# Performance work log

Hardware: AMD Instinct MI355X
Metric: run time of the kernel (lower is better)

Reference implementation:

```python
import jax, jax.numpy as jnp
import numpy as np

L, B, N, C, H = 8, 8, 512, 1024, 16
D = C // H
TP = (2.0 * D) ** 0.5  # temperature_coeff * head_dim, sqrt


def _ln(x):
    # LayerNorm(eps=1e-6, no affine)
    m = jnp.mean(x, axis=-1, keepdims=True)
    v = jnp.var(x, axis=-1, keepdims=True)
    return (x - m) * jax.lax.rsqrt(v + 1e-6)


def _modulate(x, shift, scale):
    return x * (1 + scale) + shift


def setup_inputs() -> dict:
    key = jax.random.key(0)
    ks = jax.random.split(key, 18)
    s = 0.02
    return {
        "x": jax.random.normal(ks[0], (B, N, C), dtype=jnp.float32),
        "time": jax.random.uniform(ks[1], (B, 1), dtype=jnp.float32) * 100.0,
        "label": jax.random.normal(ks[2], (B, 2), dtype=jnp.float32),
        "x_mask": jax.random.randint(ks[3], (B, N, 1), 0, 2).astype(jnp.float32),
        # ValueLabelEmbed: Linear(2 -> C)
        "Wl": jax.random.normal(ks[4], (C, 2), dtype=jnp.float32) * s,
        "bl": jnp.zeros((C,), dtype=jnp.float32),
        # per-layer stacked weights (leading dim L)
        "Wq": jax.random.normal(ks[5], (L, C, C), dtype=jnp.float32) * s,
        "Wk": jax.random.normal(ks[6], (L, C, C), dtype=jnp.float32) * s,
        "Wv": jax.random.normal(ks[7], (L, C, C), dtype=jnp.float32) * s,
        "W1": jax.random.normal(ks[8], (L, 4 * C, C), dtype=jnp.float32) * s,
        "b1": jnp.zeros((L, 4 * C), dtype=jnp.float32),
        "W2": jax.random.normal(ks[9], (L, C, 4 * C), dtype=jnp.float32) * s,
        "b2": jnp.zeros((L, C), dtype=jnp.float32),
        "Wm": jax.random.normal(ks[10], (L, 6 * C, C), dtype=jnp.float32) * s,
        "bm": jnp.zeros((L, 6 * C), dtype=jnp.float32),
        # FinalLayer
        "Wf": jax.random.normal(ks[11], (C, C), dtype=jnp.float32) * s,
        "bf": jnp.zeros((C,), dtype=jnp.float32),
        "Wmf": jax.random.normal(ks[12], (2 * C, C), dtype=jnp.float32) * s,
        "bmf": jnp.zeros((2 * C,), dtype=jnp.float32),
    }


def reference(x, time, label, x_mask, Wl, bl, Wq, Wk, Wv, W1, b1, W2, b2, Wm, bm, Wf, bf, Wmf, bmf):
    # ValueLabelEmbed: (B,2) -> (B,1,C)
    lemb = (label @ Wl.T + bl)[:, None, :]
    # TimeEmbedding: interleaved sin/cos of time / 10000^(2i/d)
    base = jnp.power(10000.0, 2.0 * jnp.arange(C, dtype=jnp.float32) / C)
    te = time / base  # (B, C)
    even = (jnp.arange(C) % 2) == 0
    te = jnp.where(even, jnp.sin(te), jnp.cos(te))
    c = lemb + te[:, None, :]  # (B,1,C)

    # self-attention mask: True where exactly one of the pair is valid
    xm = x_mask[:, :, 0]  # (B,N)
    mask = ((xm[:, :, None] + xm[:, None, :]) == 1.0)[:, None, :, :]  # (B,1,N,N)

    def block(xc, p):
        wq, wk, wv, w1, bb1, w2, bb2, wm, bbm = p
        m6 = jax.nn.selu(c) @ wm.T + bbm  # (B,1,6C)
        sm, sc, gm, sf, cf, gf = jnp.split(m6, 6, axis=-1)
        h = _modulate(_ln(xc), sm, sc) * x_mask
        q = (h @ wq.T).reshape(B, N, H, D)
        k = (h @ wk.T).reshape(B, N, H, D)
        v = (h @ wv.T).reshape(B, N, H, D)
        scores = jnp.einsum('bqhd,bkhd->bhqk', q, k) / TP
        scores = jnp.where(mask, -jnp.inf, scores)
        alpha = jax.nn.softmax(scores, axis=-1)
        att = jnp.einsum('bhqk,bkhd->bqhd', alpha, v).reshape(B, N, C)
        xc = xc + gm * att
        h2 = _modulate(_ln(xc), sf, cf)
        ffn = jax.nn.selu(h2 @ w1.T + bb1) @ w2.T + bb2
        xc = (xc + gf * ffn) * x_mask
        return xc, None

    x, _ = jax.lax.scan(block, x, (Wq, Wk, Wv, W1, b1, W2, b2, Wm, bm))

    # FinalLayer
    m2 = jax.nn.selu(c) @ Wmf.T + bmf
    shift, scale = jnp.split(m2, 2, axis=-1)
    out = (_modulate(_ln(x), shift, scale) @ Wf.T + bf) * x_mask
    return out
```

## Files before the change

kernel.cpp:

```cpp
#include <hip/hip_runtime.h>
#include <hip/hip_bf16.h>
#include <cstddef>

#define DEVI __device__ __forceinline__

typedef __attribute__((ext_vector_type(4))) float f4v;
typedef __attribute__((ext_vector_type(8))) short s8v;
typedef __attribute__((ext_vector_type(4))) short s4v;

using bf16 = __hip_bfloat16;

constexpr float SELU_A = 1.6732632423543772f;
constexpr float SELU_S = 1.0507009873554805f;
constexpr float TPINV  = 0.08838834764831845f;

DEVI float bfbits(short s) { return __uint_as_float(((unsigned)(unsigned short)s) << 16); }
DEVI unsigned short f2bu(float f) {
  bf16 h = __float2bfloat16(f);
  return __builtin_bit_cast(unsigned short, h);
}
DEVI float seluf(float x) { return x > 0.f ? SELU_S * x : SELU_S * SELU_A * (__expf(x) - 1.f); }

DEVI void gl16(const void* g, void* l) {
  __builtin_amdgcn_global_load_lds((__attribute__((address_space(1))) void*)g,
                                   (__attribute__((address_space(3))) void*)l, 16, 0, 0);
}

DEVI void conv8(const float* __restrict__ src, bf16* __restrict__ dst) {
  f4v a = *(const f4v*)src;
  f4v b = *(const f4v*)(src + 4);
  s8v o;
  #pragma unroll
  for (int j = 0; j < 4; j++) { o[j] = (short)f2bu(a[j]); o[4 + j] = (short)f2bu(b[j]); }
  *(s8v*)dst = o;
}

__global__ void k_compact(const float* __restrict__ xm, int* __restrict__ idx,
                          int* __restrict__ pos, int* __restrict__ cnt,
                          int* __restrict__ start, int* __restrict__ t2b)
{
  int t = threadIdx.x;
  int b = t >> 6, lane = t & 63;
  __shared__ int scnt[8];
  int base = b * 512 + lane * 8;
  int mb[8]; int lc = 0;
  #pragma unroll
  for (int i = 0; i < 8; i++) { mb[i] = (xm[base + i] != 0.f) ? 1 : 0; lc += mb[i]; }
  int s = lc;
  #pragma unroll
  for (int o = 1; o < 64; o <<= 1) { int tt = __shfl_up(s, o); if (lane >= o) s += tt; }
  int run = s - lc;
  #pragma unroll
  for (int i = 0; i < 8; i++) {
    int n = lane * 8 + i;
    if (mb[i]) { idx[b * 512 + run] = n; pos[b * 512 + n] = run; run++; }
    else pos[b * 512 + n] = -1;
  }
  if (lane == 63) scnt[b] = s;
  __syncthreads();
  if (t == 0) {
    int st = 0, tile = 0;
    for (int bb = 0; bb < 8; bb++) {
      cnt[bb] = scnt[bb];
      start[bb] = st;
      int nt = (scnt[bb] + 127) >> 7;
      for (int k = 0; k < nt; k++) t2b[tile++] = bb;
      st += nt * 128;
    }
    start[8] = st;
    for (; tile < 32; tile++) t2b[tile] = 0;
  }
}

__global__ __launch_bounds__(256) void k_gather(const float* __restrict__ xin,
    const int* __restrict__ idx, const int* __restrict__ cnt,
    const int* __restrict__ start, const int* __restrict__ t2b,
    float* __restrict__ xc)
{
  int row = blockIdx.x, t = threadIdx.x;
  if (row >= start[8]) return;
  int tb = t2b[row >> 7], slot = row - start[tb];
  f4v v = {0.f, 0.f, 0.f, 0.f};
  if (slot < cnt[tb])
    v = *(const f4v*)&xin[((size_t)tb * 512 + idx[tb * 512 + slot]) * 1024 + t * 4];
  *(f4v*)&xc[(size_t)row * 1024 + t * 4] = v;
}

__global__ __launch_bounds__(256) void k_scatter(const float* __restrict__ ffin,
    const int* __restrict__ pos, const int* __restrict__ start, float* __restrict__ out)
{
  int row = blockIdx.x, t = threadIdx.x, b = row >> 9;
  int p = pos[row];
  f4v v = {0.f, 0.f, 0.f, 0.f};
  if (p >= 0) v = *(const f4v*)&ffin[(size_t)(start[b] + p) * 1024 + t * 4];
  *(f4v*)&out[(size_t)row * 1024 + t * 4] = v;
}

__global__ __launch_bounds__(256) void k_convall(
    const float* __restrict__ wq, const float* __restrict__ wk, const float* __restrict__ wv,
    const float* __restrict__ w1, const float* __restrict__ w2,
    bf16* __restrict__ wqkvb, bf16* __restrict__ w1b, bf16* __restrict__ w2b)
{
  int i = blockIdx.x * 256 + threadIdx.x;
  if (i < 393216) {
    int o = i * 8;
    int row = o >> 10, col = o & 1023;
    int sel = row >> 10, sr = row & 1023;
    conv8((sel == 0 ? wq : sel == 1 ? wk : wv) + (size_t)sr * 1024 + col, wqkvb + o);
  } else if (i < 917504) {
    size_t o = (size_t)(i - 393216) * 8;
    conv8(w1 + o, w1b + o);
  } else if (i < 1441792) {
    size_t o = (size_t)(i - 917504) * 8;
    conv8(w2 + o, w2b + o);
  }
}

__global__ void k_cond(const float* __restrict__ tim, const float* __restrict__ lab,
                       const float* __restrict__ Wl, const float* __restrict__ bl,
                       float* __restrict__ cs)
{
  int b = blockIdx.x, t = threadIdx.x;
  float l0 = lab[b * 2 + 0], l1 = lab[b * 2 + 1], tv = tim[b];
  #pragma unroll
  for (int i = 0; i < 4; i++) {
    int j = t + 256 * i;
    float e = powf(10000.f, (2.f * (float)j) * (1.f / 1024.f));
    float arg = tv / e;
    float te = ((j & 1) == 0) ? sinf(arg) : cosf(arg);
    float c = l0 * Wl[j * 2 + 0] + l1 * Wl[j * 2 + 1] + bl[j] + te;
    cs[b * 1024 + j] = seluf(c);
  }
}

__global__ __launch_bounds__(256) void k_small(
    const float* __restrict__ cs, const float* __restrict__ W, const float* __restrict__ bias,
    float* __restrict__ out, int O, int mode)
{
  __shared__ float cls[8192];
  int t = threadIdx.x;
  #pragma unroll
  for (int i = 0; i < 8; i++)
    *(f4v*)&cls[i * 1024 + t * 4] = *(const f4v*)&cs[i * 1024 + t * 4];
  __syncthreads();
  int w = t >> 6, l = t & 63;
  int o = blockIdx.x * 4 + w;
  if (o >= O) return;
  float acc[8] = {0.f, 0.f, 0.f, 0.f, 0.f, 0.f, 0.f, 0.f};
  const float* Wr = W + (size_t)o * 1024;
  for (int i = 0; i < 16; i++) {
    int k = i * 64 + l;
    float wv = Wr[k];
    #pragma unroll
    for (int b = 0; b < 8; b++) acc[b] += wv * cls[b * 1024 + k];
  }
  #pragma unroll
  for (int b = 0; b < 8; b++) {
    #pragma unroll
    for (int off = 32; off; off >>= 1) acc[b] += __shfl_xor(acc[b], off);
  }
  float bv = bias[o];
  #pragma unroll
  for (int b = 0; b < 8; b++) {
    if (l == b) {
      float val = acc[b] + bv;
      size_t dst;
      if (mode == 0) { int ll = o / 6144, ft = o - ll * 6144; dst = ((size_t)ll * 8 + b) * 6144 + ft; }
      else dst = (size_t)b * 2048 + o;
      out[dst] = val;
    }
  }
}

__global__ __launch_bounds__(256) void k_lnmod(
    const float* __restrict__ x, const float* __restrict__ shiftB, const float* __restrict__ scaleB,
    int bstride, const int* __restrict__ cnt, const int* __restrict__ start,
    const int* __restrict__ t2b, bf16* __restrict__ out)
{
  int row = blockIdx.x, t = threadIdx.x;
  if (row >= start[8]) return;
  int tb = t2b[row >> 7], slot = row - start[tb];
  if (slot >= cnt[tb]) {
    s4v z = {0, 0, 0, 0};
    *(s4v*)&out[(size_t)row * 1024 + t * 4] = z;
    return;
  }
  const float* xr = x + (size_t)row * 1024;
  f4v v = *(const f4v*)&xr[t * 4];
  float s = v[0] + v[1] + v[2] + v[3];
  float ss = v[0]*v[0] + v[1]*v[1] + v[2]*v[2] + v[3]*v[3];
  #pragma unroll
  for (int off = 32; off; off >>= 1) { s += __shfl_xor(s, off); ss += __shfl_xor(ss, off); }
  __shared__ float rs[4], rss[4];
  int w = t >> 6;
  if ((t & 63) == 0) { rs[w] = s; rss[w] = ss; }
  __syncthreads();
  s = rs[0] + rs[1] + rs[2] + rs[3];
  ss = rss[0] + rss[1] + rss[2] + rss[3];
  float mean = s * (1.f / 1024.f);
  float var = ss * (1.f / 1024.f) - mean * mean;
  float rstd = rsqrtf(var + 1e-6f);
  f4v sh = *(const f4v*)&shiftB[(size_t)tb * bstride + t * 4];
  f4v sc = *(const f4v*)&scaleB[(size_t)tb * bstride + t * 4];
  s4v o;
  #pragma unroll
  for (int i = 0; i < 4; i++)
    o[i] = (short)f2bu((v[i] - mean) * rstd * (1.f + sc[i]) + sh[i]);
  *(s4v*)&out[(size_t)row * 1024 + t * 4] = o;
}

__global__ __launch_bounds__(256) void k_resid(
    float* __restrict__ x, const bf16* __restrict__ att, const float* __restrict__ m6b,
    const int* __restrict__ cnt, const int* __restrict__ start,
    const int* __restrict__ t2b, bf16* __restrict__ h2)
{
  int row = blockIdx.x, t = threadIdx.x;
  if (row >= start[8]) return;
  int tb = t2b[row >> 7], slot = row - start[tb];
  if (slot >= cnt[tb]) {
    s4v z = {0, 0, 0, 0};
    *(s4v*)&h2[(size_t)row * 1024 + t * 4] = z;
    return;
  }
  float* xr = x + (size_t)row * 1024;
  const float* gm = m6b + (size_t)tb * 6144 + 2048;
  const float* sf = m6b + (size_t)tb * 6144 + 3072;
  const float* cf = m6b + (size_t)tb * 6144 + 4096;
  f4v xv = *(const f4v*)&xr[t * 4];
  s4v av = *(const s4v*)&att[((size_t)tb * 512 + slot) * 1024 + t * 4];
  f4v gv = *(const f4v*)&gm[t * 4];
  f4v vv;
  #pragma unroll
  for (int i = 0; i < 4; i++) vv[i] = xv[i] + gv[i] * bfbits(av[i]);
  *(f4v*)&xr[t * 4] = vv;
  float s = vv[0] + vv[1] + vv[2] + vv[3];
  float ss = vv[0]*vv[0] + vv[1]*vv[1] + vv[2]*vv[2] + vv[3]*vv[3];
  #pragma unroll
  for (int off = 32; off; off >>= 1) { s += __shfl_xor(s, off); ss += __shfl_xor(ss, off); }
  __shared__ float rs[4], rss[4];
  int w = t >> 6;
  if ((t & 63) == 0) { rs[w] = s; rss[w] = ss; }
  __syncthreads();
  s = rs[0] + rs[1] + rs[2] + rs[3];
  ss = rss[0] + rss[1] + rss[2] + rss[3];
  float mean = s * (1.f / 1024.f);
  float var = ss * (1.f / 1024.f) - mean * mean;
  float rstd = rsqrtf(var + 1e-6f);
  f4v sfv = *(const f4v*)&sf[t * 4];
  f4v cfv = *(const f4v*)&cf[t * 4];
  s4v o;
  #pragma unroll
  for (int i = 0; i < 4; i++)
    o[i] = (short)f2bu((vv[i] - mean) * rstd * (1.f + cfv[i]) + sfv[i]);
  *(s4v*)&h2[(size_t)row * 1024 + t * 4] = o;
}

__global__ __launch_bounds__(256) void k_attn(
    const bf16* __restrict__ q, const bf16* __restrict__ k, const bf16* __restrict__ vt,
    const int* __restrict__ cnt, bf16* __restrict__ att,
    const float* __restrict__ nwq, const float* __restrict__ nwk, const float* __restrict__ nwv,
    const float* __restrict__ nw1, const float* __restrict__ nw2,
    bf16* __restrict__ dqkv, bf16* __restrict__ dw1, bf16* __restrict__ dw2, int mode)
{
  if (blockIdx.x >= 4) {
    int cid = (blockIdx.x - 4) * 128 + blockIdx.y;
    int i0 = cid * 256 + threadIdx.x;
    #pragma unroll
    for (int half = 0; half < 2; half++) {
      int j = i0 * 2 + half;
      if (mode == 1) {
        if (j < 131072) conv8(nwq + (size_t)j * 8, dqkv + (size_t)j * 8);
      } else {
        if (j < 393216) {
          int o = j * 8;
          int row = o >> 10, col = o & 1023;
          int sel = row >> 10, sr = row & 1023;
          conv8((sel == 0 ? nwq : sel == 1 ? nwk : nwv) + (size_t)sr * 1024 + col, dqkv + o);
        } else if (j < 917504) {
          size_t o = (size_t)(j - 393216) * 8;
          conv8(nw1 + o, dw1 + o);
        } else {
          size_t o = (size_t)(j - 917504) * 8;
          conv8(nw2 + o, dw2 + o);
        }
      }
    }
    return;
  }

  int bh = blockIdx.y, b = bh >> 4, hh = bh & 15;
  int cntb = cnt[b];
  if ((int)blockIdx.x * 128 >= cntb) return;
  int t = threadIdx.x, w = t >> 6, lane = t & 63;
  int fr = lane & 15, g = lane >> 4;
  int qw = blockIdx.x * 128 + w * 32;
  const size_t ho = (size_t)bh * (512 * 64);

  __shared__ bf16 Pb[4][32][72];

  s8v qf[2][2];
  #pragma unroll
  for (int mf = 0; mf < 2; mf++)
    #pragma unroll
    for (int kk = 0; kk < 2; kk++)
      qf[mf][kk] = *(const s8v*)(q + ho + (size_t)(qw + mf * 16 + fr) * 64 + kk * 32 + g * 8);

  float mrow[2][4], lsum[2][4];
  f4v oacc[2][4];
  const f4v vzero = {0.f, 0.f, 0.f, 0.f};
  #pragma unroll
  for (int mf = 0; mf < 2; mf++)
    #pragma unroll
    for (int r = 0; r < 4; r++) { mrow[mf][r] = -3.0e38f; lsum[mf][r] = 0.f; }
  #pragma unroll
  for (int mf = 0; mf < 2; mf++)
    #pragma unroll
    for (int nd = 0; nd < 4; nd++) oacc[mf][nd] = vzero;

  int nkt = (cntb + 63) >> 6;
  for (int kt = 0; kt < nkt; kt++) {
    int kb0 = kt * 64;
    f4v sacc[2][4];
    #pragma unroll
    for (int mf = 0; mf < 2; mf++)
      #pragma unroll
      for (int nf = 0; nf < 4; nf++) sacc[mf][nf] = vzero;
    #pragma unroll
    for (int kk = 0; kk < 2; kk++) {
      s8v kf[4];
      #pragma unroll
      for (int nf = 0; nf < 4; nf++)
        kf[nf] = *(const s8v*)(k + ho + (size_t)(kb0 + nf * 16 + fr) * 64 + kk * 32 + g * 8);
      #pragma unroll
      for (int mf = 0; mf < 2; mf++)
        #pragma unroll
        for (int nf = 0; nf < 4; nf++)
          sacc[mf][nf] = __builtin_amdgcn_mfma_f32_16x16x32_bf16(qf[mf][kk], kf[nf], sacc[mf][nf], 0, 0, 0);
    }
    #pragma unroll
    for (int mf = 0; mf < 2; mf++) {
      #pragma unroll
      for (int r = 0; r < 4; r++) {
        float mx = -3.0e38f;
        #pragma unroll
        for (int nf = 0; nf < 4; nf++) {
          float s = sacc[mf][nf][r] * TPINV;
          if (kb0 + nf * 16 + fr >= cntb) s = -1.0e30f;
          sacc[mf][nf][r] = s;
          mx = fmaxf(mx, s);
        }
        mx = fmaxf(mx, __shfl_xor(mx, 1));
        mx = fmaxf(mx, __shfl_xor(mx, 2));
        mx = fmaxf(mx, __shfl_xor(mx, 4));
        mx = fmaxf(mx, __shfl_xor(mx, 8));
        float mnew = fmaxf(mrow[mf][r], mx);
        float corr = __expf(mrow[mf][r] - mnew);
        mrow[mf][r] = mnew;
        float ps = 0.f;
        #pragma unroll
        for (int nf = 0; nf < 4; nf++) {
          float p = __expf(sacc[mf][nf][r] - mnew);
          ps += p;
          Pb[w][mf * 16 + g * 4 + r][nf * 16 + fr] = __float2bfloat16(p);
        }
        lsum[mf][r] = lsum[mf][r] * corr + ps;
        #pragma unroll
        for (int nd = 0; nd < 4; nd++) oacc[mf][nd][r] *= corr;
      }
    }
    #pragma unroll
    for (int kk = 0; kk < 2; kk++) {
      s8v pf[2], vf[4];
      #pragma unroll
      for (int mf = 0; mf < 2; mf++)
        pf[mf] = *(const s8v*)&Pb[w][mf * 16 + fr][kk * 32 + g * 8];
      #pragma unroll
      for (int nd = 0; nd < 4; nd++)
        vf[nd] = *(const s8v*)(vt + ho + (size_t)(nd * 16 + fr) * 512 + kb0 + kk * 32 + g * 8);
      #pragma unroll
      for (int mf = 0; mf < 2; mf++)
        #pragma unroll
        for (int nd = 0; nd < 4; nd++)
          oacc[mf][nd] = __builtin_amdgcn_mfma_f32_16x16x32_bf16(pf[mf], vf[nd], oacc[mf][nd], 0, 0, 0);
    }
  }
  float inv[2][4];
  #pragma unroll
  for (int mf = 0; mf < 2; mf++)
    #pragma unroll
    for (int r = 0; r < 4; r++) {
      float ls = lsum[mf][r];
      ls += __shfl_xor(ls, 1);
      ls += __shfl_xor(ls, 2);
      ls += __shfl_xor(ls, 4);
      ls += __shfl_xor(ls, 8);
      inv[mf][r] = 1.f / ls;
    }
  #pragma unroll
  for (int mf = 0; mf < 2; mf++)
    #pragma unroll
    for (int nd = 0; nd < 4; nd++)
      #pragma unroll
      for (int r = 0; r < 4; r++) {
        int row = qw + mf * 16 + g * 4 + r;
        att[(size_t)(b * 512 + row) * 1024 + hh * 64 + nd * 16 + fr] =
            __float2bfloat16(oacc[mf][nd][r] * inv[mf][r]);
      }
}

template <int EPI, int BN>
__global__ __launch_bounds__(256) void k_gemm(
    const bf16* __restrict__ A, const bf16* __restrict__ W,
    const float* __restrict__ bias, int Kst, int kLen, int Ncols,
    const int* __restrict__ cnt, const int* __restrict__ start, const int* __restrict__ t2b,
    bf16* __restrict__ outb, float* __restrict__ outf)
{
  constexpr int FN = BN / 32;
  constexpr int NW = BN / 32;
  __shared__ bf16 As[128][64];
  __shared__ bf16 Ws[BN][64];
  int t = threadIdx.x, lane = t & 63, w = t >> 6;
  int wr = w >> 1, wc = w & 1;
  int m0 = blockIdx.y * 128, n0 = blockIdx.x * BN;
  if (m0 >= start[8]) return;
  int kOff = blockIdx.z * kLen;
  int fr = lane & 15, g = lane >> 4;

  const bf16* Abase = A + (size_t)m0 * Kst + kOff;
  const bf16* Wbase = W + (size_t)n0 * Kst + kOff;

  const f4v vzero = {0.f, 0.f, 0.f, 0.f};
  f4v acc[4][FN];
  #pragma unroll
  for (int i = 0; i < 4; i++)
    #pragma unroll
    for (int j = 0; j < FN; j++) acc[i][j] = vzero;

  int nkt = kLen >> 6;
  for (int kt = 0; kt < nkt; kt++) {
    int k0 = kt << 6;
    __syncthreads();
    #pragma unroll
    for (int i = 0; i < 4; i++) {
      int off = w * 4096 + i * 1024 + lane * 16;
      int row = off >> 7, ce = (off & 127) >> 1;
      gl16(Abase + (size_t)row * Kst + k0 + ce, (char*)As + w * 4096 + i * 1024);
    }
    #pragma unroll
    for (int i = 0; i < NW; i++) {
      int off = w * (NW * 1024) + i * 1024 + lane * 16;
      int row = off >> 7, ce = (off & 127) >> 1;
      gl16(Wbase + (size_t)row * Kst + k0 + ce, (char*)Ws + w * (NW * 1024) + i * 1024);
    }
    __syncthreads();
    #pragma unroll
    for (int kk = 0; kk < 2; kk++) {
      s8v af[4], bfr[FN];
      #pragma unroll
      for (int mf = 0; mf < 4; mf++)
        af[mf] = *(const s8v*)&As[wr * 64 + mf * 16 + fr][kk * 32 + g * 8];
      #pragma unroll
      for (int nf = 0; nf < FN; nf++)
        bfr[nf] = *(const s8v*)&Ws[wc * (BN / 2) + nf * 16 + fr][kk * 32 + g * 8];
      #pragma unroll
      for (int mf = 0; mf < 4; mf++)
        #pragma unroll
        for (int nf = 0; nf < FN; nf++)
          acc[mf][nf] = __builtin_amdgcn_mfma_f32_16x16x32_bf16(af[mf], bfr[nf], acc[mf][nf], 0, 0, 0);
    }
  }

  int tb = t2b[m0 >> 7];
  int sb = start[tb];
  int rq = (lane >> 4) * 4;
  #pragma unroll
  for (int mf = 0; mf < 4; mf++) {
    #pragma unroll
    for (int nf = 0; nf < FN; nf++) {
      int row0 = m0 + wr * 64 + mf * 16 + rq;
      int col = n0 + wc * (BN / 2) + nf * 16 + fr;
      if (EPI == 0) {
        int sel = col >> 10, cl = col & 1023;
        int nn = row0 - sb;
        int h2 = cl >> 6, dd = cl & 63;
        if (sel == 2) {
          s4v o4;
          #pragma unroll
          for (int r = 0; r < 4; r++) o4[r] = (short)f2bu(acc[mf][nf][r]);
          *(s4v*)&outb[(size_t)2 * 4194304 + (((size_t)tb * 16 + h2) * 64 + dd) * 512 + nn] = o4;
        } else {
          #pragma unroll
          for (int r = 0; r < 4; r++)
            outb[(size_t)sel * 4194304 + (((size_t)tb * 16 + h2) * 512 + (nn + r)) * 64 + dd] =
                __float2bfloat16(acc[mf][nf][r]);
        }
      } else {
        #pragma unroll
        for (int r = 0; r < 4; r++) {
          int row = row0 + r;
          float val = acc[mf][nf][r];
          if (EPI == 1) {
            outb[(size_t)row * Ncols + col] = __float2bfloat16(seluf(val + bias[col]));
          } else if (EPI == 3) {
            outf[(size_t)row * 1024 + col] = val + bias[col];
          } else {
            outb[(size_t)blockIdx.z * 4194304 + (size_t)row * 1024 + col] = __float2bfloat16(val);
          }
        }
      }
    }
  }
}

__global__ __launch_bounds__(256) void k_comb(
    const bf16* __restrict__ part, const float* __restrict__ bias,
    const float* __restrict__ gfb, const float* __restrict__ shiftN,
    const float* __restrict__ scaleN, int strideN,
    float* __restrict__ x, const int* __restrict__ cnt, const int* __restrict__ start,
    const int* __restrict__ t2b, bf16* __restrict__ h)
{
  int row = blockIdx.x, t = threadIdx.x;
  if (row >= start[8]) return;
  int tb = t2b[row >> 7], slot = row - start[tb];
  if (slot >= cnt[tb]) return;
  size_t o = (size_t)row * 1024 + t * 4;
  f4v sum = {0.f, 0.f, 0.f, 0.f};
  #pragma unroll
  for (int p = 0; p < 8; p++) {
    s4v pv = *(const s4v*)&part[o + (size_t)p * 4194304];
    #pragma unroll
    for (int i = 0; i < 4; i++) sum[i] += bfbits(pv[i]);
  }
  f4v bv = *(const f4v*)&bias[t * 4];
  f4v gf = *(const f4v*)&gfb[(size_t)tb * 6144 + t * 4];
  f4v xv = *(const f4v*)&x[o];
  f4v vv;
  #pragma unroll
  for (int i = 0; i < 4; i++)
    vv[i] = xv[i] + gf[i] * (sum[i] + bv[i]);
  *(f4v*)&x[o] = vv;
  float s = vv[0] + vv[1] + vv[2] + vv[3];
  float ss = vv[0]*vv[0] + vv[1]*vv[1] + vv[2]*vv[2] + vv[3]*vv[3];
  #pragma unroll
  for (int off = 32; off; off >>= 1) { s += __shfl_xor(s, off); ss += __shfl_xor(ss, off); }
  __shared__ float rs[4], rss[4];
  int w = t >> 6;
  if ((t & 63) == 0) { rs[w] = s; rss[w] = ss; }
  __syncthreads();
  s = rs[0] + rs[1] + rs[2] + rs[3];
  ss = rss[0] + rss[1] + rss[2] + rss[3];
  float mean = s * (1.f / 1024.f);
  float var = ss * (1.f / 1024.f) - mean * mean;
  float rstd = rsqrtf(var + 1e-6f);
  f4v sh = *(const f4v*)&shiftN[(size_t)tb * strideN + t * 4];
  f4v sc = *(const f4v*)&scaleN[(size_t)tb * strideN + t * 4];
  s4v ho;
  #pragma unroll
  for (int i = 0; i < 4; i++)
    ho[i] = (short)f2bu((vv[i] - mean) * rstd * (1.f + sc[i]) + sh[i]);
  *(s4v*)&h[(size_t)row * 1024 + t * 4] = ho;
}

extern "C" void kernel_launch(void* const* d_in, const int* in_sizes, int n_in,
                              void* d_out, int out_size, void* d_ws, size_t ws_size,
                              hipStream_t stream)
{
  const float* x_in  = (const float*)d_in[0];
  const float* tim   = (const float*)d_in[1];
  const float* lab   = (const float*)d_in[2];
  const float* xmask = (const float*)d_in[3];
  const float* Wl  = (const float*)d_in[4];
  const float* bl  = (const float*)d_in[5];
  const float* Wq  = (const float*)d_in[6];
  const float* Wk  = (const float*)d_in[7];
  const float* Wv  = (const float*)d_in[8];
  const float* W1  = (const float*)d_in[9];
  const float* b1  = (const float*)d_in[10];
  const float* W2  = (const float*)d_in[11];
  const float* b2  = (const float*)d_in[12];
  const float* Wm  = (const float*)d_in[13];
  const float* bm  = (const float*)d_in[14];
  const float* Wf  = (const float*)d_in[15];
  const float* bfp = (const float*)d_in[16];
  const float* Wmf = (const float*)d_in[17];
  const float* bmf = (const float*)d_in[18];

  char* ws = (char*)d_ws;
  float* x     = (float*)(ws + 0);
  float* cs    = (float*)(ws + 16777216);
  float* mAll  = (float*)(ws + 16809984);
  float* m2v   = (float*)(ws + 18382848);
  bf16*  h     = (bf16*)(ws + 18448384);
  bf16*  qb    = (bf16*)(ws + 26836992);
  bf16*  kb    = (bf16*)(ws + 35225600);
  bf16*  vb    = (bf16*)(ws + 43614208);
  bf16*  att   = (bf16*)(ws + 52002816);
  bf16*  f1    = (bf16*)(ws + 60391424);
  bf16*  wqkv0 = (bf16*)(ws + 93945856);
  bf16*  w1b0  = (bf16*)(ws + 100237312);
  bf16*  w2b0  = (bf16*)(ws + 108625920);
  bf16*  wfb   = (bf16*)(ws + 117014528);
  float* ffin  = (float*)(ws + 119111680);
  int*   idxb  = (int*)(ws + 135888896);
  int*   posb  = (int*)(ws + 135905280);
  int*   cntb  = (int*)(ws + 135921664);
  int*   strtb = (int*)(ws + 135921728);
  int*   t2bb  = (int*)(ws + 135921792);
  bf16*  wqkv1 = (bf16*)(ws + 135921920);
  bf16*  w1b1  = (bf16*)(ws + 142213376);
  bf16*  w2b1  = (bf16*)(ws + 150601984);
  bf16*  part  = (bf16*)(ws + 158990592);

  bf16* wqkvS[2] = { wqkv0, wqkv1 };
  bf16* w1S[2]   = { w1b0, w1b1 };
  bf16* w2S[2]   = { w2b0, w2b1 };

  k_compact<<<1, 512, 0, stream>>>(xmask, idxb, posb, cntb, strtb, t2bb);
  k_gather<<<4096, 256, 0, stream>>>(x_in, idxb, cntb, strtb, t2bb, x);

  k_cond<<<8, 256, 0, stream>>>(tim, lab, Wl, bl, cs);
  k_small<<<12288, 256, 0, stream>>>(cs, Wm, bm, mAll, 49152, 0);
  k_small<<<512, 256, 0, stream>>>(cs, Wmf, bmf, m2v, 2048, 1);

  k_convall<<<5632, 256, 0, stream>>>(Wq, Wk, Wv, W1, W2, wqkv0, w1b0, w2b0);
  k_lnmod<<<4096, 256, 0, stream>>>(x, mAll + 0, mAll + 1024, 6144, cntb, strtb, t2bb, h);

  for (int l = 0; l < 8; l++) {
    const float* m6b = mAll + (size_t)l * 49152;
    int sel = l & 1, nsel = sel ^ 1;
    int last = (l == 7);

    k_gemm<0, 64><<<dim3(48, 32), 256, 0, stream>>>(h, wqkvS[sel], nullptr, 1024, 1024, 3072,
                                                    cntb, strtb, t2bb, qb, nullptr);
    if (!last) {
      k_attn<<<dim3(26, 128), 256, 0, stream>>>(qb, kb, vb, cntb, att,
          Wq + (size_t)(l + 1) * 1048576, Wk + (size_t)(l + 1) * 1048576,
          Wv + (size_t)(l + 1) * 1048576, W1 + (size_t)(l + 1) * 4194304,
          W2 + (size_t)(l + 1) * 4194304,
          wqkvS[nsel], w1S[nsel], w2S[nsel], 0);
    } else {
      k_attn<<<dim3(26, 128), 256, 0, stream>>>(qb, kb, vb, cntb, att,
          Wf, Wf, Wf, Wf, Wf, wfb, wfb, wfb, 1);
    }
    k_resid<<<4096, 256, 0, stream>>>(x, att, m6b, cntb, strtb, t2bb, h);
    k_gemm<1, 64><<<dim3(64, 32), 256, 0, stream>>>(h, w1S[sel], b1 + l * 4096, 1024, 1024, 4096,
                                                    cntb, strtb, t2bb, f1, nullptr);
    k_gemm<4, 128><<<dim3(8, 32, 8), 256, 0, stream>>>(f1, w2S[sel], nullptr, 4096, 512, 1024,
                                                       cntb, strtb, t2bb, part, nullptr);
    const float* nShift = last ? m2v : (mAll + (size_t)(l + 1) * 49152);
    const float* nScale = last ? (m2v + 1024) : (mAll + (size_t)(l + 1) * 49152 + 1024);
    int nStride = last ? 2048 : 6144;
    k_comb<<<4096, 256, 0, stream>>>(part, b2 + l * 1024, m6b + 5120,
                                     nShift, nScale, nStride,
                                     x, cntb, strtb, t2bb, h);
  }

  k_gemm<3, 64><<<dim3(16, 32), 256, 0, stream>>>(h, wfb, bfp, 1024, 1024, 1024,
                                                  cntb, strtb, t2bb, nullptr, ffin);
  k_scatter<<<4096, 256, 0, stream>>>(ffin, posb, strtb, (float*)d_out);
}
```

Measured before the change: 1.500 ms.

## Switch GEMM to 32x32x16 MFMA with XOR-swizzled LDS tiles

The generic GEMM kernel now issues 32x32x16 bf16 MFMA instructions instead of 16x16x32, so each wave handles two 32-row fragments per N fragment. LDS tiles are stored with an XOR swizzle on 16-byte slots, keyed by row, both when filling from global memory and when reading fragments, to avoid bank conflicts. The epilogue is remapped to the 32x32 accumulator layout (four quads of four rows). This aims to cut LDS read conflicts and per-FLOP instruction overhead. The risk is mis-mapping the output or swizzle layout, and BN must be a multiple of 64.

```diff
diff --git a/kernel.cpp b/kernel.cpp
--- a/kernel.cpp
+++ b/kernel.cpp
@@ -5,6 +5,7 @@
 #define DEVI __device__ __forceinline__
 
 typedef __attribute__((ext_vector_type(4))) float f4v;
+typedef __attribute__((ext_vector_type(16))) float f16v;
 typedef __attribute__((ext_vector_type(8))) short s8v;
 typedef __attribute__((ext_vector_type(4))) short s4v;
 
@@ -415,8 +416,8 @@
     const int* __restrict__ cnt, const int* __restrict__ start, const int* __restrict__ t2b,
     bf16* __restrict__ outb, float* __restrict__ outf)
 {
-  constexpr int FN = BN / 32;
-  constexpr int NW = BN / 32;
+  constexpr int NFR = BN / 64;
+  constexpr int NW  = BN / 32;
   __shared__ bf16 As[128][64];
   __shared__ bf16 Ws[BN][64];
   int t = threadIdx.x, lane = t & 63, w = t >> 6;
@@ -424,17 +425,18 @@
   int m0 = blockIdx.y * 128, n0 = blockIdx.x * BN;
   if (m0 >= start[8]) return;
   int kOff = blockIdx.z * kLen;
-  int fr = lane & 15, g = lane >> 4;
+  int r32 = lane & 31, hi = lane >> 5;
 
   const bf16* Abase = A + (size_t)m0 * Kst + kOff;
   const bf16* Wbase = W + (size_t)n0 * Kst + kOff;
 
-  const f4v vzero = {0.f, 0.f, 0.f, 0.f};
-  f4v acc[4][FN];
-  #pragma unroll
-  for (int i = 0; i < 4; i++)
-    #pragma unroll
-    for (int j = 0; j < FN; j++) acc[i][j] = vzero;
+  f16v acc[2][NFR];
+  #pragma unroll
+  for (int i = 0; i < 2; i++)
+    #pragma unroll
+    for (int j = 0; j < NFR; j++)
+      #pragma unroll
+      for (int e = 0; e < 16; e++) acc[i][j][e] = 0.f;
 
   int nkt = kLen >> 6;
   for (int kt = 0; kt < nkt; kt++) {
@@ -442,69 +444,79 @@
     __syncthreads();
     #pragma unroll
     for (int i = 0; i < 4; i++) {
-      int off = w * 4096 + i * 1024 + lane * 16;
-      int row = off >> 7, ce = (off & 127) >> 1;
-      gl16(Abase + (size_t)row * Kst + k0 + ce, (char*)As + w * 4096 + i * 1024);
+      int Z = w * 4096 + i * 1024 + lane * 16;
+      int row = Z >> 7, slot = (Z >> 4) & 7;
+      int ss = slot ^ (row & 7);
+      gl16(Abase + (size_t)row * Kst + k0 + ss * 8, (char*)As + Z);
     }
     #pragma unroll
     for (int i = 0; i < NW; i++) {
-      int off = w * (NW * 1024) + i * 1024 + lane * 16;
-      int row = off >> 7, ce = (off & 127) >> 1;
-      gl16(Wbase + (size_t)row * Kst + k0 + ce, (char*)Ws + w * (NW * 1024) + i * 1024);
+      int Z = w * (NW * 1024) + i * 1024 + lane * 16;
+      int row = Z >> 7, slot = (Z >> 4) & 7;
+      int ss = slot ^ (row & 7);
+      gl16(Wbase + (size_t)row * Kst + k0 + ss * 8, (char*)Ws + Z);
     }
     __syncthreads();
     #pragma unroll
-    for (int kk = 0; kk < 2; kk++) {
-      s8v af[4], bfr[FN];
-      #pragma unroll
-      for (int mf = 0; mf < 4; mf++)
-        af[mf] = *(const s8v*)&As[wr * 64 + mf * 16 + fr][kk * 32 + g * 8];
-      #pragma unroll
-      for (int nf = 0; nf < FN; nf++)
-        bfr[nf] = *(const s8v*)&Ws[wc * (BN / 2) + nf * 16 + fr][kk * 32 + g * 8];
-      #pragma unroll
-      for (int mf = 0; mf < 4; mf++)
+    for (int kk = 0; kk < 4; kk++) {
+      s8v af[2], bfr[NFR];
+      #pragma unroll
+      for (int mf = 0; mf < 2; mf++) {
+        int row = wr * 64 + mf * 32 + r32;
+        int sl = (kk * 2 + hi) ^ (row & 7);
+        af[mf] = *(const s8v*)((const char*)As + row * 128 + sl * 16);
+      }
+      #pragma unroll
+      for (int nf = 0; nf < NFR; nf++) {
+        int row = wc * (BN / 2) + nf * 32 + r32;
+        int sl = (kk * 2 + hi) ^ (row & 7);
+        bfr[nf] = *(const s8v*)((const char*)Ws + row * 128 + sl * 16);
+      }
+      #pragma unroll
+      for (int mf = 0; mf < 2; mf++)
         #pragma unroll
-        for (int nf = 0; nf < FN; nf++)
-          acc[mf][nf] = __builtin_amdgcn_mfma_f32_16x16x32_bf16(af[mf], bfr[nf], acc[mf][nf], 0, 0, 0);
+        for (int nf = 0; nf < NFR; nf++)
+          acc[mf][nf] = __builtin_amdgcn_mfma_f32_32x32x16_bf16(af[mf], bfr[nf], acc[mf][nf], 0, 0, 0);
     }
   }
 
   int tb = t2b[m0 >> 7];
   int sb = start[tb];
-  int rq = (lane >> 4) * 4;
-  #pragma unroll
-  for (int mf = 0; mf < 4; mf++) {
-    #pragma unroll
-    for (int nf = 0; nf < FN; nf++) {
-      int row0 = m0 + wr * 64 + mf * 16 + rq;
-      int col = n0 + wc * (BN / 2) + nf * 16 + fr;
-      if (EPI == 0) {
-        int sel = col >> 10, cl = col & 1023;
-        int nn = row0 - sb;
-        int h2 = cl >> 6, dd = cl & 63;
-        if (sel == 2) {
-          s4v o4;
-          #pragma unroll
-          for (int r = 0; r < 4; r++) o4[r] = (short)f2bu(acc[mf][nf][r]);
-          *(s4v*)&outb[(size_t)2 * 4194304 + (((size_t)tb * 16 + h2) * 64 + dd) * 512 + nn] = o4;
+  #pragma unroll
+  for (int mf = 0; mf < 2; mf++) {
+    #pragma unroll
+    for (int nf = 0; nf < NFR; nf++) {
+      int col = n0 + wc * (BN / 2) + nf * 32 + r32;
+      #pragma unroll
+      for (int qd = 0; qd < 4; qd++) {
+        int row0 = m0 + wr * 64 + mf * 32 + qd * 8 + hi * 4;
+        if (EPI == 0) {
+          int sel = col >> 10, cl = col & 1023;
+          int nn = row0 - sb;
+          int h2 = cl >> 6, dd = cl & 63;
+          if (sel == 2) {
+            s4v o4;
+            #pragma unroll
+            for (int r = 0; r < 4; r++) o4[r] = (short)f2bu(acc[mf][nf][qd * 4 + r]);
+            *(s4v*)&outb[(size_t)2 * 4194304 + (((size_t)tb * 16 + h2) * 64 + dd) * 512 + nn] = o4;
+          } else {
+            #pragma unroll
+            for (int r = 0; r < 4; r++)
+              outb[(size_t)sel * 4194304 + (((size_t)tb * 16 + h2) * 512 + (nn + r)) * 64 + dd] =
+                  __float2bfloat16(acc[mf][nf][qd * 4 + r]);
+          }
         } else {
           #pragma unroll
-          for (int r = 0; r < 4; r++)
-            outb[(size_t)sel * 4194304 + (((size_t)tb * 16 + h2) * 512 + (nn + r)) * 64 + dd] =
-                __float2bfloat16(acc[mf][nf][r]);
-        }
-      } else {
-        #pragma unroll
-        for (int r = 0; r < 4; r++) {
-          int row = row0 + r;
-          float val = acc[mf][nf][r];
-          if (EPI == 1) {
-            outb[(size_t)row * Ncols + col] = __float2bfloat16(seluf(val + bias[col]));
-          } else if (EPI == 3) {
-            outf[(size_t)row * 1024 + col] = val + bias[col];
-          } else {
-            outb[(size_t)blockIdx.z * 4194304 + (size_t)row * 1024 + col] = __float2bfloat16(val);
+          for (int r = 0; r < 4; r++) {
+            int row = row0 + r;
+            float val = acc[mf][nf][qd * 4 + r];
+            if (EPI == 1) {
+              outb[(size_t)row * Ncols + col] = __float2bfloat16(seluf(val + bias[col]));
+            } else if (EPI == 3) {
+              outf[(size_t)row * 1024 + col] = val + bias[col];
+            } else {
+              outb[(size_t)blockIdx.z * 4194304 + (size_t)row * 1024 + col] = __float2bfloat16(val);
+            }
           }
         }
       }
```

After: 1.366 ms. 8.9% less time.
